# Performance work log

Hardware: AMD Instinct MI355X
Metric: run time of the kernel (lower is better)

## Reference

```python
import jax, jax.numpy as jnp
import numpy as np

# ---- config (mirrors the repo-level globals) ----
B, N = 8, 1024                 # batch, points per cloud
SHAPE_SIZE = 256               # per-point shape-code width
HEAD = 8                       # point_size + 1 - shape_size passthrough channels
SC_HID = 256                   # shape_code_encoder_hidden_dims = [256]
SC_OUT = 128                   # shape_code_encoder_output_size
E = 16                         # num_categories
INTER = HEAD + SC_OUT          # 136
ENC_DIMS = [INTER, 256, 512]   # encoder_hidden_dims
LATENT = 1024                  # latent_size
DEC_DIMS = [LATENT, 1024, 2048]
MAX_PTS, PSI = 1024, 7         # max_num_points, point_size_intermediate
DEC_OUT = (PSI + 1) * MAX_PTS  # 8192


def setup_inputs() -> dict:
    key = jax.random.key(0)
    ks = jax.random.split(key, 20)
    s = 0.02
    inp = {
        'x': jax.random.normal(ks[0], (B, HEAD + SHAPE_SIZE, N), jnp.float32),
        'cats': jax.random.randint(ks[1], (B, N), 0, E),
        # per-category shape encoders: Linear(256->256) ReLU Linear(256->128)
        'W1': jax.random.normal(ks[2], (E, SHAPE_SIZE, SC_HID), jnp.float32) * s,
        'b1': jnp.zeros((E, SC_HID), jnp.float32),
        'W2': jax.random.normal(ks[3], (E, SC_HID, SC_OUT), jnp.float32) * s,
        'b2': jnp.zeros((E, SC_OUT), jnp.float32),
        # pointwise Conv1d stack 136->256->512->1024 (weights [out,in])
        'Wc1': jax.random.normal(ks[4], (ENC_DIMS[1], ENC_DIMS[0]), jnp.float32) * s,
        'bc1': jnp.zeros((ENC_DIMS[1],), jnp.float32),
        'Wc2': jax.random.normal(ks[5], (ENC_DIMS[2], ENC_DIMS[1]), jnp.float32) * s,
        'bc2': jnp.zeros((ENC_DIMS[2],), jnp.float32),
        'Wc3': jax.random.normal(ks[6], (LATENT, ENC_DIMS[2]), jnp.float32) * s,
        'bc3': jnp.zeros((LATENT,), jnp.float32),
        # decoder MLP 1024->1024->2048->8192 (weights [in,out])
        'Wd1': jax.random.normal(ks[7], (DEC_DIMS[0], DEC_DIMS[1]), jnp.float32) * s,
        'bd1': jnp.zeros((DEC_DIMS[1],), jnp.float32),
        'Wd2': jax.random.normal(ks[8], (DEC_DIMS[1], DEC_DIMS[2]), jnp.float32) * s,
        'bd2': jnp.zeros((DEC_DIMS[2],), jnp.float32),
        'Wd3': jax.random.normal(ks[9], (DEC_DIMS[2], DEC_OUT), jnp.float32) * s,
        'bd3': jnp.zeros((DEC_OUT,), jnp.float32),
    }
    return inp


def reference(x, cats, W1, b1, W2, b2, Wc1, bc1, Wc2, bc2, Wc3, bc3,
              Wd1, bd1, Wd2, bd2, Wd3, bd3):
    # ---- encoder: category-routed per-point shape MLP ----
    sf = jnp.swapaxes(x[:, -SHAPE_SIZE:, :], 1, 2)      # [B, N, 256]
    mask = jax.nn.one_hot(cats, E, dtype=x.dtype)       # [B, N, E]
    routed = jnp.zeros((B, N, SC_OUT), x.dtype)
    for e in range(E):  # fixed small expert loop; avoids [B,N,E,hid] blowup
        h = jax.nn.relu(sf @ W1[e] + b1[e])             # [B, N, 256]
        o = h @ W2[e] + b2[e]                           # [B, N, 128]
        routed = routed + mask[..., e:e + 1] * o
    xi = jnp.concatenate([x[:, :HEAD, :], jnp.swapaxes(routed, 1, 2)], axis=1)  # [B,136,N]
    # ---- pointwise conv stack + max pool ----
    h = jax.nn.relu(jnp.einsum('oc,bcn->bon', Wc1, xi) + bc1[:, None])
    h = jax.nn.relu(jnp.einsum('oc,bcn->bon', Wc2, h) + bc2[:, None])
    h = jnp.einsum('oc,bcn->bon', Wc3, h) + bc3[:, None]  # [B, 1024, N]
    latent = jnp.max(h, axis=2)                            # [B, 1024]
    # ---- decoder MLP ----
    d = jax.nn.relu(latent @ Wd1 + bd1)
    d = jax.nn.relu(d @ Wd2 + bd2)
    out = (d @ Wd3 + bd3).reshape(B, MAX_PTS, PSI + 1)     # [B, 1024, 8]
    return out, latent
```

## Files before the change

kernel.cpp:

```cpp
#include <hip/hip_runtime.h>
#include <math.h>

#define BB 8
#define NN 1024
#define HEADC 8
#define SS 256
#define SCO 128
#define NE 16
#define C1 256
#define C2 512
#define C3 1024
#define NPTS (BB*NN)
#define XCH (HEADC+SS)
#define K1P 192
#define BK 64

typedef unsigned short ushortT;
typedef __attribute__((ext_vector_type(8))) short bf16x8;
typedef __attribute__((ext_vector_type(4))) float f32x4;

#define OB_XTB   0ull
#define OB_HB    4325376ull
#define OB_H2    0ull
#define OB_XI    8519680ull
#define OB_H1    11665408ull
#define OB_WT1   15859712ull
#define OB_WT2   15958016ull
#define OB_WT3   16220160ull
#define OB_W1T   17268736ull
#define OB_W2T   19365888ull
#define OB_PMAX  20414464ull
#define OB_LAT   20676608ull
#define OB_D1    20709376ull
#define OB_D2    20742144ull
#define OB_DPART 20807680ull
#define OB_IDX   22904832ull
#define OB_OFFS  22937600ull

__device__ __forceinline__ ushortT f2b(float f) {
  unsigned u = __float_as_uint(f);
  return (ushortT)((u + 0x7FFFu + ((u >> 16) & 1u)) >> 16);
}

__global__ __launch_bounds__(256) void k_prep_x(
    const float* __restrict__ x, ushortT* __restrict__ xTb, ushortT* __restrict__ xi) {
  __shared__ float t[32][33];
  int b = blockIdx.z;
  int n0 = blockIdx.x * 32, c0 = blockIdx.y * 32;
  int tx = threadIdx.x & 31, ty = threadIdx.x >> 5;
  const float* s = x + (size_t)b * XCH * NN;
  for (int yy = ty; yy < 32; yy += 8) {
    int c = c0 + yy;
    if (c < XCH) t[yy][tx] = s[(size_t)c * NN + n0 + tx];
  }
  __syncthreads();
  for (int yy = ty; yy < 32; yy += 8) {
    int n = n0 + yy, c = c0 + tx;
    if (c < XCH) {
      ushortT v = f2b(t[tx][yy]);
      xTb[(size_t)(b * NN + n) * XCH + c] = v;
      if (c < HEADC) xi[(size_t)(b * NN + n) * K1P + c] = v;
    }
  }
}

__global__ __launch_bounds__(256) void k_zero_xi(ushortT* __restrict__ xi) {
  int i = blockIdx.x * 256 + threadIdx.x;
  if (i >= NPTS * 56) return;
  int p = i / 56, c = 136 + i % 56;
  xi[(size_t)p * K1P + c] = 0;
}

__global__ __launch_bounds__(256) void k_cvt_pad(
    const float* __restrict__ src, ushortT* __restrict__ dst, int cs, int cd, int total) {
  int i = blockIdx.x * 256 + threadIdx.x;
  if (i >= total) return;
  int r = i / cd, c = i % cd;
  dst[i] = (c < cs) ? f2b(src[(size_t)r * cs + c]) : (ushortT)0;
}

__global__ __launch_bounds__(256) void k_transpose_wb(
    const float* __restrict__ src, ushortT* __restrict__ dst, int R, int C,
    size_t sBS, size_t dBS) {
  __shared__ float t[32][33];
  const float* s = src + (size_t)blockIdx.z * sBS;
  ushortT* d = dst + (size_t)blockIdx.z * dBS;
  int r0 = blockIdx.y * 32, c0 = blockIdx.x * 32;
  int tx = threadIdx.x & 31, ty = threadIdx.x >> 5;
  for (int yy = ty; yy < 32; yy += 8) {
    int r = r0 + yy, c = c0 + tx;
    if (r < R && c < C) t[yy][tx] = s[(size_t)r * C + c];
  }
  __syncthreads();
  for (int yy = ty; yy < 32; yy += 8) {
    int c = c0 + yy, r = r0 + tx;
    if (r < R && c < C) d[(size_t)c * R + r] = f2b(t[tx][yy]);
  }
}

__global__ __launch_bounds__(1024) void k_bucket(
    const int* __restrict__ cats, int* __restrict__ idx, int* __restrict__ offs) {
  __shared__ int cnt[NE];
  __shared__ int base[NE + 1];
  __shared__ int cur[NE];
  int tid = threadIdx.x;
  if (tid < NE) cnt[tid] = 0;
  __syncthreads();
  for (int p = tid; p < NPTS; p += 1024) atomicAdd(&cnt[cats[p]], 1);
  __syncthreads();
  if (tid == 0) {
    int s = 0;
    for (int e = 0; e < NE; ++e) { base[e] = s; cur[e] = s; s += cnt[e]; }
    base[NE] = s;
  }
  __syncthreads();
  for (int p = tid; p < NPTS; p += 1024) {
    int pos = atomicAdd(&cur[cats[p]], 1);
    idx[pos] = p;
  }
  if (tid <= NE) offs[tid] = base[tid];
}

template<int MODE>
__global__ __launch_bounds__(256) void k_gemm(
    const ushortT* __restrict__ A, int lda,
    const ushortT* __restrict__ Bt, int ldb,
    const float* __restrict__ bias,
    ushortT* __restrict__ Cb, int ldc,
    float* __restrict__ pmaxOut,
    const int* __restrict__ idx, const int* __restrict__ offsp,
    int K, int relu) {
  __shared__ ushortT As[128 * BK];
  __shared__ ushortT Bs[128 * BK];
  __shared__ int pts[128];
  __shared__ float smax[2][128];
  int tid = threadIdx.x;
  int wave = tid >> 6, lane = tid & 63;
  int wm = wave >> 1, wn = wave & 1;
  int g = lane >> 4, lr = lane & 15;
  int n0 = blockIdx.x * 128;
  int m0 = 0, nr = 128, bucket0 = 0;

  if constexpr (MODE == 2 || MODE == 3) {
    int e = blockIdx.y, t = blockIdx.z;
    int s0 = offsp[e];
    int cnt = offsp[e + 1] - s0;
    int p0 = t * 128;
    if (p0 >= cnt) return;
    nr = min(128, cnt - p0);
    bucket0 = s0 + p0;
    Bt += (size_t)e * ((MODE == 2) ? 256 * 256 : 128 * 256);
    bias += e * ((MODE == 2) ? 256 : 128);
    if (tid < 128) pts[tid] = (tid < nr) ? idx[bucket0 + tid] : 0;
  } else {
    m0 = blockIdx.y * 128;
  }

  f32x4 acc[4][4];
#pragma unroll
  for (int mi = 0; mi < 4; ++mi)
#pragma unroll
    for (int nj = 0; nj < 4; ++nj) acc[mi][nj] = (f32x4)(0.f);

  int nkt = K / BK;
  for (int kt = 0; kt < nkt; ++kt) {
    int k0 = kt * BK;
    __syncthreads();
#pragma unroll
    for (int i = 0; i < 4; ++i) {
      int c = tid + i * 256;
      int row = c >> 3, slot = c & 7;
      int ss = slot ^ (row & 7);
      uint4 v;
      if constexpr (MODE == 2) {
        if (row < nr) v = *(const uint4*)(A + (size_t)pts[row] * lda + 8 + k0 + slot * 8);
        else { v.x = v.y = v.z = v.w = 0u; }
      } else if constexpr (MODE == 3) {
        if (row < nr) v = *(const uint4*)(A + (size_t)(bucket0 + row) * lda + k0 + slot * 8);
        else { v.x = v.y = v.z = v.w = 0u; }
      } else {
        v = *(const uint4*)(A + (size_t)(m0 + row) * lda + k0 + slot * 8);
      }
      *(uint4*)(As + row * BK + ss * 8) = v;
      uint4 w = *(const uint4*)(Bt + (size_t)(n0 + row) * ldb + k0 + slot * 8);
      *(uint4*)(Bs + row * BK + ss * 8) = w;
    }
    __syncthreads();
#pragma unroll
    for (int kk = 0; kk < 2; ++kk) {
      bf16x8 av[4], bv[4];
#pragma unroll
      for (int mi = 0; mi < 4; ++mi) {
        int row = wm * 64 + mi * 16 + lr;
        int slot = (kk * 4 + g) ^ (row & 7);
        av[mi] = *(const bf16x8*)(As + row * BK + slot * 8);
      }
#pragma unroll
      for (int nj = 0; nj < 4; ++nj) {
        int row = wn * 64 + nj * 16 + lr;
        int slot = (kk * 4 + g) ^ (row & 7);
        bv[nj] = *(const bf16x8*)(Bs + row * BK + slot * 8);
      }
#pragma unroll
      for (int mi = 0; mi < 4; ++mi)
#pragma unroll
        for (int nj = 0; nj < 4; ++nj)
          acc[mi][nj] = __builtin_amdgcn_mfma_f32_16x16x32_bf16(av[mi], bv[nj], acc[mi][nj], 0, 0, 0);
    }
  }

  if constexpr (MODE == 1) {
#pragma unroll
    for (int nj = 0; nj < 4; ++nj) {
      float m = -INFINITY;
#pragma unroll
      for (int mi = 0; mi < 4; ++mi)
#pragma unroll
        for (int r = 0; r < 4; ++r) m = fmaxf(m, acc[mi][nj][r]);
      m = fmaxf(m, __shfl_xor(m, 16));
      m = fmaxf(m, __shfl_xor(m, 32));
      if (lane < 16) smax[wm][wn * 64 + nj * 16 + lr] = m;
    }
    __syncthreads();
    if (tid < 128) {
      float m = fmaxf(smax[0][tid], smax[1][tid]);
      pmaxOut[(size_t)blockIdx.y * C3 + n0 + tid] = m + bias[n0 + tid];
    }
  } else {
#pragma unroll
    for (int mi = 0; mi < 4; ++mi)
#pragma unroll
      for (int nj = 0; nj < 4; ++nj)
#pragma unroll
        for (int r = 0; r < 4; ++r) {
          int lrow = wm * 64 + mi * 16 + g * 4 + r;
          int col = n0 + wn * 64 + nj * 16 + lr;
          float v = acc[mi][nj][r] + bias[col];
          if (relu) v = fmaxf(v, 0.f);
          ushortT b = f2b(v);
          if constexpr (MODE == 0) {
            Cb[(size_t)(m0 + lrow) * ldc + col] = b;
          } else if constexpr (MODE == 2) {
            if (lrow < nr) Cb[(size_t)(bucket0 + lrow) * ldc + col] = b;
          } else {
            if (lrow < nr) Cb[(size_t)pts[lrow] * ldc + 8 + col] = b;
          }
        }
  }
}

__global__ __launch_bounds__(256) void k_latmax(
    const float* __restrict__ pmax, float* __restrict__ lat, float* __restrict__ outLat) {
  int id = blockIdx.x * 256 + threadIdx.x;
  int b = id >> 10, o = id & 1023;
  float m = -INFINITY;
  for (int t = 0; t < 8; ++t)
    m = fmaxf(m, pmax[(size_t)((b << 3) + t) * C3 + o]);
  lat[id] = m;
  outLat[id] = m;
}

__global__ __launch_bounds__(256) void k_gemm_part(
    const float* __restrict__ A, const float* __restrict__ W,
    float* __restrict__ part, int K, int Ncol, int chunkLog) {
  __shared__ float a[8][256];
  int chunk = 1 << chunkLog;
  int i0 = blockIdx.y << chunkLog;
  int j = blockIdx.x * 256 + threadIdx.x;
  for (int k = threadIdx.x; k < 8 * chunk; k += 256) {
    int r = k >> chunkLog, i = k & (chunk - 1);
    a[r][i] = A[(size_t)r * K + i0 + i];
  }
  __syncthreads();
  float acc[8];
#pragma unroll
  for (int r = 0; r < 8; ++r) acc[r] = 0.f;
  const float* wp = W + (size_t)i0 * Ncol + j;
  for (int i4 = 0; i4 < (chunk >> 2); ++i4) {
    float w0 = wp[(size_t)(4 * i4 + 0) * Ncol];
    float w1 = wp[(size_t)(4 * i4 + 1) * Ncol];
    float w2 = wp[(size_t)(4 * i4 + 2) * Ncol];
    float w3 = wp[(size_t)(4 * i4 + 3) * Ncol];
#pragma unroll
    for (int r = 0; r < 8; ++r) {
      float4 av = ((const float4*)a[r])[i4];
      acc[r] += av.x * w0 + av.y * w1 + av.z * w2 + av.w * w3;
    }
  }
#pragma unroll
  for (int r = 0; r < 8; ++r)
    part[((size_t)(blockIdx.y * 8 + r)) * Ncol + j] = acc[r];
}

__global__ __launch_bounds__(256) void k_reduce(
    const float* __restrict__ part, const float* __restrict__ bias,
    float* __restrict__ out, int ncolLog, int KC, int doRelu) {
  int o = blockIdx.x * 256 + threadIdx.x;
  int j = o & ((1 << ncolLog) - 1);
  float s = bias[j];
  for (int kc = 0; kc < KC; ++kc)
    s += part[((size_t)kc << (ncolLog + 3)) + o];
  if (doRelu) s = fmaxf(s, 0.f);
  out[o] = s;
}

extern "C" void kernel_launch(void* const* d_in, const int* in_sizes, int n_in,
                              void* d_out, int out_size, void* d_ws, size_t ws_size,
                              hipStream_t stream) {
  const float* x    = (const float*)d_in[0];
  const int*   cats = (const int*)d_in[1];
  const float* W1   = (const float*)d_in[2];
  const float* b1   = (const float*)d_in[3];
  const float* W2   = (const float*)d_in[4];
  const float* b2   = (const float*)d_in[5];
  const float* Wc1  = (const float*)d_in[6];
  const float* bc1  = (const float*)d_in[7];
  const float* Wc2  = (const float*)d_in[8];
  const float* bc2  = (const float*)d_in[9];
  const float* Wc3  = (const float*)d_in[10];
  const float* bc3  = (const float*)d_in[11];
  const float* Wd1  = (const float*)d_in[12];
  const float* bd1  = (const float*)d_in[13];
  const float* Wd2  = (const float*)d_in[14];
  const float* bd2  = (const float*)d_in[15];
  const float* Wd3  = (const float*)d_in[16];
  const float* bd3  = (const float*)d_in[17];
  float* out = (float*)d_out;

  char* wsb = (char*)d_ws;
  ushortT* xTb  = (ushortT*)(wsb + OB_XTB);
  ushortT* hB   = (ushortT*)(wsb + OB_HB);
  ushortT* h2   = (ushortT*)(wsb + OB_H2);
  ushortT* xi   = (ushortT*)(wsb + OB_XI);
  ushortT* h1   = (ushortT*)(wsb + OB_H1);
  ushortT* Wt1b = (ushortT*)(wsb + OB_WT1);
  ushortT* Wt2b = (ushortT*)(wsb + OB_WT2);
  ushortT* Wt3b = (ushortT*)(wsb + OB_WT3);
  ushortT* W1tb = (ushortT*)(wsb + OB_W1T);
  ushortT* W2tb = (ushortT*)(wsb + OB_W2T);
  float* pmax   = (float*)(wsb + OB_PMAX);
  float* lat    = (float*)(wsb + OB_LAT);
  float* d1w    = (float*)(wsb + OB_D1);
  float* d2w    = (float*)(wsb + OB_D2);
  float* dpart  = (float*)(wsb + OB_DPART);
  int*   idx    = (int*)(wsb + OB_IDX);
  int*   offs   = (int*)(wsb + OB_OFFS);

  k_prep_x<<<dim3(32, 9, BB), 256, 0, stream>>>(x, xTb, xi);
  k_zero_xi<<<(NPTS * 56 + 255) / 256, 256, 0, stream>>>(xi);
  k_cvt_pad<<<(256 * K1P + 255) / 256, 256, 0, stream>>>(Wc1, Wt1b, 136, K1P, 256 * K1P);
  k_cvt_pad<<<(512 * 256 + 255) / 256, 256, 0, stream>>>(Wc2, Wt2b, 256, 256, 512 * 256);
  k_cvt_pad<<<(1024 * 512 + 255) / 256, 256, 0, stream>>>(Wc3, Wt3b, 512, 512, 1024 * 512);
  k_transpose_wb<<<dim3(8, 8, NE), 256, 0, stream>>>(W1, W1tb, 256, 256, 65536, 65536);
  k_transpose_wb<<<dim3(4, 8, NE), 256, 0, stream>>>(W2, W2tb, 256, 128, 32768, 32768);

  k_bucket<<<1, 1024, 0, stream>>>(cats, idx, offs);
  k_gemm<2><<<dim3(2, NE, 8), 256, 0, stream>>>(xTb, XCH, W1tb, 256, b1, hB, 256,
                                                nullptr, idx, offs, 256, 1);
  k_gemm<3><<<dim3(1, NE, 8), 256, 0, stream>>>(hB, 256, W2tb, 256, b2, xi, K1P,
                                                nullptr, idx, offs, 256, 0);

  k_gemm<0><<<dim3(2, 64), 256, 0, stream>>>(xi, K1P, Wt1b, K1P, bc1, h1, 256,
                                             nullptr, nullptr, nullptr, K1P, 1);
  k_gemm<0><<<dim3(4, 64), 256, 0, stream>>>(h1, 256, Wt2b, 256, bc2, h2, 512,
                                             nullptr, nullptr, nullptr, 256, 1);
  k_gemm<1><<<dim3(8, 64), 256, 0, stream>>>(h2, 512, Wt3b, 512, bc3, nullptr, 0,
                                             pmax, nullptr, nullptr, 512, 0);
  k_latmax<<<32, 256, 0, stream>>>(pmax, lat, out + 65536);

  k_gemm_part<<<dim3(4, 32), 256, 0, stream>>>(lat, Wd1, dpart, 1024, 1024, 5);
  k_reduce<<<32, 256, 0, stream>>>(dpart, bd1, d1w, 10, 32, 1);
  k_gemm_part<<<dim3(8, 16), 256, 0, stream>>>(d1w, Wd2, dpart, 1024, 2048, 6);
  k_reduce<<<64, 256, 0, stream>>>(dpart, bd2, d2w, 11, 16, 1);
  k_gemm_part<<<dim3(32, 8), 256, 0, stream>>>(d2w, Wd3, dpart, 2048, 8192, 8);
  k_reduce<<<256, 256, 0, stream>>>(dpart, bd3, out, 13, 8, 0);
  (void)in_sizes; (void)n_in; (void)out_size; (void)ws_size;
}
```

Baseline: 311.6 us.

## Vectorize decoder GEMV and reductions and merge weight-prep kernels

Rewrites the decoder split-K GEMV so each thread loads and accumulates float4 columns, with re-tuned chunk sizes and block sizes. The partial-sum reduce and latent max-pool kernels also move to float4 loads and stores. The three Conv1d weight conversions become one kernel, and the two expert-weight transposes become another, which cuts launch count. The kernel that zeroed the xi padding columns is dropped, so those columns rely on whatever the workspace already holds. The workspace index offsets move to make room for the larger partial buffer.

```diff
diff --git a/kernel.cpp b/kernel.cpp
--- a/kernel.cpp
+++ b/kernel.cpp
@@ -34,8 +34,8 @@
 #define OB_D1    20709376ull
 #define OB_D2    20742144ull
 #define OB_DPART 20807680ull
-#define OB_IDX   22904832ull
-#define OB_OFFS  22937600ull
+#define OB_IDX   25001984ull
+#define OB_OFFS  25034752ull
 
 __device__ __forceinline__ ushortT f2b(float f) {
   unsigned u = __float_as_uint(f);
@@ -64,37 +64,50 @@
   }
 }
 
-__global__ __launch_bounds__(256) void k_zero_xi(ushortT* __restrict__ xi) {
+#define CW_S1 (256*192)
+#define CW_S2 (512*256)
+#define CW_S3 (1024*512)
+__global__ __launch_bounds__(256) void k_cvt_weights(
+    const float* __restrict__ Wc1, const float* __restrict__ Wc2,
+    const float* __restrict__ Wc3, ushortT* __restrict__ w1,
+    ushortT* __restrict__ w2, ushortT* __restrict__ w3) {
   int i = blockIdx.x * 256 + threadIdx.x;
-  if (i >= NPTS * 56) return;
-  int p = i / 56, c = 136 + i % 56;
-  xi[(size_t)p * K1P + c] = 0;
-}
-
-__global__ __launch_bounds__(256) void k_cvt_pad(
-    const float* __restrict__ src, ushortT* __restrict__ dst, int cs, int cd, int total) {
-  int i = blockIdx.x * 256 + threadIdx.x;
-  if (i >= total) return;
-  int r = i / cd, c = i % cd;
-  dst[i] = (c < cs) ? f2b(src[(size_t)r * cs + c]) : (ushortT)0;
-}
-
-__global__ __launch_bounds__(256) void k_transpose_wb(
-    const float* __restrict__ src, ushortT* __restrict__ dst, int R, int C,
-    size_t sBS, size_t dBS) {
+  if (i < CW_S1) {
+    int r = i / K1P, c = i - r * K1P;
+    w1[i] = (c < 136) ? f2b(Wc1[(size_t)r * 136 + c]) : (ushortT)0;
+  } else if (i < CW_S1 + CW_S2) {
+    int k = i - CW_S1;
+    w2[k] = f2b(Wc2[k]);
+  } else if (i < CW_S1 + CW_S2 + CW_S3) {
+    int k = i - CW_S1 - CW_S2;
+    w3[k] = f2b(Wc3[k]);
+  }
+}
+
+__global__ __launch_bounds__(256) void k_transpose_w12(
+    const float* __restrict__ W1, const float* __restrict__ W2,
+    ushortT* __restrict__ W1tb, ushortT* __restrict__ W2tb) {
   __shared__ float t[32][33];
-  const float* s = src + (size_t)blockIdx.z * sBS;
-  ushortT* d = dst + (size_t)blockIdx.z * dBS;
+  int z = blockIdx.z;
+  const float* s;
+  ushortT* d;
+  int C;
+  if (z < 16) { s = W1 + (size_t)z * 65536; d = W1tb + (size_t)z * 65536; C = 256; }
+  else {
+    if (blockIdx.x >= 4) return;
+    s = W2 + (size_t)(z - 16) * 32768; d = W2tb + (size_t)(z - 16) * 32768; C = 128;
+  }
+  const int R = 256;
   int r0 = blockIdx.y * 32, c0 = blockIdx.x * 32;
   int tx = threadIdx.x & 31, ty = threadIdx.x >> 5;
   for (int yy = ty; yy < 32; yy += 8) {
     int r = r0 + yy, c = c0 + tx;
-    if (r < R && c < C) t[yy][tx] = s[(size_t)r * C + c];
+    if (c < C) t[yy][tx] = s[(size_t)r * C + c];
   }
   __syncthreads();
   for (int yy = ty; yy < 32; yy += 8) {
     int c = c0 + yy, r = r0 + tx;
-    if (r < R && c < C) d[(size_t)c * R + r] = f2b(t[tx][yy]);
+    if (c < C) d[(size_t)c * R + r] = f2b(t[tx][yy]);
   }
 }
 
@@ -251,57 +264,66 @@
 
 __global__ __launch_bounds__(256) void k_latmax(
     const float* __restrict__ pmax, float* __restrict__ lat, float* __restrict__ outLat) {
-  int id = blockIdx.x * 256 + threadIdx.x;
-  int b = id >> 10, o = id & 1023;
-  float m = -INFINITY;
-  for (int t = 0; t < 8; ++t)
-    m = fmaxf(m, pmax[(size_t)((b << 3) + t) * C3 + o]);
-  lat[id] = m;
-  outLat[id] = m;
-}
-
-__global__ __launch_bounds__(256) void k_gemm_part(
+  int id4 = blockIdx.x * 256 + threadIdx.x;
+  int b = id4 >> 8, o4 = id4 & 255;
+  f32x4 m = (f32x4)(-INFINITY);
+  for (int t = 0; t < 8; ++t) {
+    f32x4 v = *(const f32x4*)(pmax + (size_t)((b << 3) + t) * C3 + o4 * 4);
+#pragma unroll
+    for (int r = 0; r < 4; ++r) m[r] = fmaxf(m[r], v[r]);
+  }
+  *(f32x4*)(lat + (size_t)id4 * 4) = m;
+  *(f32x4*)(outLat + (size_t)id4 * 4) = m;
+}
+
+__global__ __launch_bounds__(256) void k_dec_part(
     const float* __restrict__ A, const float* __restrict__ W,
-    float* __restrict__ part, int K, int Ncol, int chunkLog) {
-  __shared__ float a[8][256];
+    float* __restrict__ part, int K, int N, int chunkLog) {
+  __shared__ float a[8 * 128];
   int chunk = 1 << chunkLog;
   int i0 = blockIdx.y << chunkLog;
-  int j = blockIdx.x * 256 + threadIdx.x;
-  for (int k = threadIdx.x; k < 8 * chunk; k += 256) {
-    int r = k >> chunkLog, i = k & (chunk - 1);
-    a[r][i] = A[(size_t)r * K + i0 + i];
-  }
-  __syncthreads();
-  float acc[8];
-#pragma unroll
-  for (int r = 0; r < 8; ++r) acc[r] = 0.f;
-  const float* wp = W + (size_t)i0 * Ncol + j;
-  for (int i4 = 0; i4 < (chunk >> 2); ++i4) {
-    float w0 = wp[(size_t)(4 * i4 + 0) * Ncol];
-    float w1 = wp[(size_t)(4 * i4 + 1) * Ncol];
-    float w2 = wp[(size_t)(4 * i4 + 2) * Ncol];
-    float w3 = wp[(size_t)(4 * i4 + 3) * Ncol];
+  int tid = threadIdx.x;
+  for (int idx = tid; idx < (8 << chunkLog); idx += blockDim.x) {
+    int r = idx >> chunkLog, i = idx & (chunk - 1);
+    a[idx] = A[(size_t)r * K + i0 + i];
+  }
+  __syncthreads();
+  int col = (blockIdx.x * blockDim.x + tid) * 4;
+  f32x4 acc[8];
+#pragma unroll
+  for (int r = 0; r < 8; ++r) acc[r] = (f32x4)(0.f);
+  const float* wp = W + (size_t)i0 * N + col;
+#pragma unroll 2
+  for (int k = 0; k < chunk; k += 4) {
+    f32x4 w0 = *(const f32x4*)(wp + (size_t)(k + 0) * N);
+    f32x4 w1 = *(const f32x4*)(wp + (size_t)(k + 1) * N);
+    f32x4 w2 = *(const f32x4*)(wp + (size_t)(k + 2) * N);
+    f32x4 w3 = *(const f32x4*)(wp + (size_t)(k + 3) * N);
 #pragma unroll
     for (int r = 0; r < 8; ++r) {
-      float4 av = ((const float4*)a[r])[i4];
-      acc[r] += av.x * w0 + av.y * w1 + av.z * w2 + av.w * w3;
-    }
-  }
-#pragma unroll
-  for (int r = 0; r < 8; ++r)
-    part[((size_t)(blockIdx.y * 8 + r)) * Ncol + j] = acc[r];
-}
-
-__global__ __launch_bounds__(256) void k_reduce(
+      const float* ar = &a[(r << chunkLog) + k];
+      acc[r] += ar[0] * w0 + ar[1] * w1 + ar[2] * w2 + ar[3] * w3;
+    }
+  }
+  float* pp = part + (size_t)(blockIdx.y * 8) * N + col;
+#pragma unroll
+  for (int r = 0; r < 8; ++r) *(f32x4*)(pp + (size_t)r * N) = acc[r];
+}
+
+__global__ __launch_bounds__(256) void k_reduce4(
     const float* __restrict__ part, const float* __restrict__ bias,
-    float* __restrict__ out, int ncolLog, int KC, int doRelu) {
-  int o = blockIdx.x * 256 + threadIdx.x;
-  int j = o & ((1 << ncolLog) - 1);
-  float s = bias[j];
+    float* __restrict__ out, int N, int KC, int doRelu) {
+  int o4 = blockIdx.x * 256 + threadIdx.x;
+  int col4 = o4 & ((N >> 2) - 1);
+  f32x4 s = ((const f32x4*)bias)[col4];
+  const f32x4* p4 = (const f32x4*)part;
   for (int kc = 0; kc < KC; ++kc)
-    s += part[((size_t)kc << (ncolLog + 3)) + o];
-  if (doRelu) s = fmaxf(s, 0.f);
-  out[o] = s;
+    s += p4[(size_t)kc * 2 * N + o4];
+  if (doRelu) {
+#pragma unroll
+    for (int r = 0; r < 4; ++r) s[r] = fmaxf(s[r], 0.f);
+  }
+  ((f32x4*)out)[o4] = s;
 }
 
 extern "C" void kernel_launch(void* const* d_in, const int* in_sizes, int n_in,
@@ -347,12 +369,9 @@
   int*   offs   = (int*)(wsb + OB_OFFS);
 
   k_prep_x<<<dim3(32, 9, BB), 256, 0, stream>>>(x, xTb, xi);
-  k_zero_xi<<<(NPTS * 56 + 255) / 256, 256, 0, stream>>>(xi);
-  k_cvt_pad<<<(256 * K1P + 255) / 256, 256, 0, stream>>>(Wc1, Wt1b, 136, K1P, 256 * K1P);
-  k_cvt_pad<<<(512 * 256 + 255) / 256, 256, 0, stream>>>(Wc2, Wt2b, 256, 256, 512 * 256);
-  k_cvt_pad<<<(1024 * 512 + 255) / 256, 256, 0, stream>>>(Wc3, Wt3b, 512, 512, 1024 * 512);
-  k_transpose_wb<<<dim3(8, 8, NE), 256, 0, stream>>>(W1, W1tb, 256, 256, 65536, 65536);
-  k_transpose_wb<<<dim3(4, 8, NE), 256, 0, stream>>>(W2, W2tb, 256, 128, 32768, 32768);
+  k_cvt_weights<<<(CW_S1 + CW_S2 + CW_S3 + 255) / 256, 256, 0, stream>>>(
+      Wc1, Wc2, Wc3, Wt1b, Wt2b, Wt3b);
+  k_transpose_w12<<<dim3(8, 8, 32), 256, 0, stream>>>(W1, W2, W1tb, W2tb);
 
   k_bucket<<<1, 1024, 0, stream>>>(cats, idx, offs);
   k_gemm<2><<<dim3(2, NE, 8), 256, 0, stream>>>(xTb, XCH, W1tb, 256, b1, hB, 256,
@@ -366,13 +385,13 @@
                                              nullptr, nullptr, nullptr, 256, 1);
   k_gemm<1><<<dim3(8, 64), 256, 0, stream>>>(h2, 512, Wt3b, 512, bc3, nullptr, 0,
                                              pmax, nullptr, nullptr, 512, 0);
-  k_latmax<<<32, 256, 0, stream>>>(pmax, lat, out + 65536);
-
-  k_gemm_part<<<dim3(4, 32), 256, 0, stream>>>(lat, Wd1, dpart, 1024, 1024, 5);
-  k_reduce<<<32, 256, 0, stream>>>(dpart, bd1, d1w, 10, 32, 1);
-  k_gemm_part<<<dim3(8, 16), 256, 0, stream>>>(d1w, Wd2, dpart, 1024, 2048, 6);
-  k_reduce<<<64, 256, 0, stream>>>(dpart, bd2, d2w, 11, 16, 1);
-  k_gemm_part<<<dim3(32, 8), 256, 0, stream>>>(d2w, Wd3, dpart, 2048, 8192, 8);
-  k_reduce<<<256, 256, 0, stream>>>(dpart, bd3, out, 13, 8, 0);
+  k_latmax<<<8, 256, 0, stream>>>(pmax, lat, out + 65536);
+
+  k_dec_part<<<dim3(4, 32), 64, 0, stream>>>(lat, Wd1, dpart, 1024, 1024, 5);
+  k_reduce4<<<8, 256, 0, stream>>>(dpart, bd1, d1w, 1024, 32, 1);
+  k_dec_part<<<dim3(8, 32), 64, 0, stream>>>(d1w, Wd2, dpart, 1024, 2048, 5);
+  k_reduce4<<<16, 256, 0, stream>>>(dpart, bd2, d2w, 2048, 32, 1);
+  k_dec_part<<<dim3(8, 16), 256, 0, stream>>>(d2w, Wd3, dpart, 2048, 8192, 7);
+  k_reduce4<<<64, 256, 0, stream>>>(dpart, bd3, out, 8192, 16, 0);
   (void)in_sizes; (void)n_in; (void)out_size; (void)ws_size;
 }
```

New measurement: 306.6 us. Within noise of the previous version (-1.6%).
